# Optimization experiments

Measured on AMD Instinct MI355X. Metric: run time of the kernel, lower is better.

The kernel has to match this reference:

```python
import jax, jax.numpy as jnp
import numpy as np


def setup_inputs() -> dict:
    key = jax.random.key(0)
    ks = jax.random.split(key, 6)
    B, L, N, C, D = 8, 512, 2048, 1024, 128
    return {
        "teacher_logits": jax.random.normal(ks[0], (B, L, N), dtype=jnp.float32),
        "teacher_features": jax.random.normal(ks[1], (B, N, C), dtype=jnp.float32),
        "Wq": jax.random.normal(ks[2], (D, C), dtype=jnp.float32) * (1.0 / np.sqrt(C)),
        "bq": jnp.zeros((D,), dtype=jnp.float32),
        "Wk": jax.random.normal(ks[3], (D, C), dtype=jnp.float32) * (1.0 / np.sqrt(C)),
        "bk": jnp.zeros((D,), dtype=jnp.float32),
    }


def reference(teacher_logits, teacher_features, Wq, bq, Wk, bk):
    # Linear projections (torch nn.Linear: x @ W^T + b)
    query = jnp.einsum("bnc,dc->bnd", teacher_features, Wq) + bq  # [B,N,D]
    key = jnp.einsum("bnc,dc->bnd", teacher_features, Wk) + bk    # [B,N,D]
    energy = jnp.einsum("bnd,bmd->bnm", query, key)               # [B,N,N]
    attention = jax.nn.softmax(energy, axis=-1)                   # softmax over last dim
    # x_m = teacher_logits @ attention^T : [B,L,N] x [B,N,N]^T -> [B,L,N]
    x_m = jnp.einsum("bln,bmn->blm", teacher_logits, attention)
    return x_m
```

## Files before the change

### kernel.cpp

```cpp
#include <hip/hip_runtime.h>
#include <hip/hip_bf16.h>

#define B_ 8
#define L_ 512
#define N_ 2048
#define C_ 1024
#define D_ 128

typedef __attribute__((ext_vector_type(8))) short    short8;
typedef __attribute__((ext_vector_type(4))) short    short4v;
typedef __attribute__((ext_vector_type(8))) _Float16 half8;
typedef __attribute__((ext_vector_type(4))) float    floatx4;

static __device__ __forceinline__ float s2f(short s) {
    return __uint_as_float(((unsigned)(unsigned short)s) << 16);
}
static __device__ __forceinline__ short f2bf(float f) {
    union { __hip_bfloat16 h; short s; } u;
    u.h = __float2bfloat16(f);
    return u.s;
}

struct F8 { float v[8]; };

static __device__ __forceinline__ F8 load8(const void* raw, long off, int is_bf16) {
    F8 r;
    if (is_bf16) {
        short8 x = *reinterpret_cast<const short8*>((const short*)raw + off);
        #pragma unroll
        for (int i = 0; i < 8; ++i) r.v[i] = s2f(x[i]);
    } else {
        const float* p = (const float*)raw + off;
        float4 a = *reinterpret_cast<const float4*>(p);
        float4 b = *reinterpret_cast<const float4*>(p + 4);
        r.v[0]=a.x; r.v[1]=a.y; r.v[2]=a.z; r.v[3]=a.w;
        r.v[4]=b.x; r.v[5]=b.y; r.v[6]=b.z; r.v[7]=b.w;
    }
    return r;
}

static __device__ __forceinline__ float bias_at(const void* raw, int d, int is_bf16) {
    return is_bf16 ? s2f(((const short*)raw)[d]) : ((const float*)raw)[d];
}

static __device__ __forceinline__ void load_lds16(const void* g, void* l) {
    __builtin_amdgcn_global_load_lds(
        (const __attribute__((address_space(1))) void*)g,
        (__attribute__((address_space(3))) void*)l, 16, 0, 0);
}

__global__ void detect_kernel(const unsigned* __restrict__ words, int* __restrict__ flag) {
    int cnt = 0;
    for (int i = threadIdx.x; i < 256; i += 64) {
        float lowv = __uint_as_float(words[i] << 16);
        float a = fabsf(lowv);
        if (a >= 1e-5f && a <= 100.0f) cnt++;
    }
    #pragma unroll
    for (int off = 32; off; off >>= 1) cnt += __shfl_down(cnt, off);
    if (threadIdx.x == 0) flag[0] = (cnt > 128) ? 1 : 0;
}

__global__ __launch_bounds__(256) void cvt_kernel(const void* __restrict__ in_raw,
                                                  short* __restrict__ out, long n,
                                                  const int* __restrict__ flag) {
    if (*flag) return;
    long i = ((long)blockIdx.x * 256 + threadIdx.x) * 8;
    if (i >= n) return;
    F8 x = load8(in_raw, i, 0);
    short8 o;
    #pragma unroll
    for (int j = 0; j < 8; ++j) o[j] = f2bf(x.v[j]);
    *reinterpret_cast<short8*>(out + i) = o;
}

__global__ __launch_bounds__(256) void cvt_half_kernel(const void* __restrict__ in_raw,
                                                       _Float16* __restrict__ out, long n,
                                                       const int* __restrict__ flag) {
    if (*flag) return;
    long i = ((long)blockIdx.x * 256 + threadIdx.x) * 8;
    if (i >= n) return;
    F8 x = load8(in_raw, i, 0);
    half8 o;
    #pragma unroll
    for (int j = 0; j < 8; ++j) o[j] = (_Float16)x.v[j];
    *reinterpret_cast<half8*>(out + i) = o;
}

__global__ __launch_bounds__(512) void proj_kernel(
    const void* __restrict__ Fraw,
    const void* __restrict__ Wq_raw, const void* __restrict__ Wk_raw,
    const _Float16* __restrict__ Wq_h, const _Float16* __restrict__ Wk_h,
    const void* __restrict__ bq_raw, const void* __restrict__ bk_raw,
    _Float16* __restrict__ Q, _Float16* __restrict__ K,
    const int* __restrict__ flag)
{
    const int is_bf16 = *flag;
    const int tid  = threadIdx.x;
    const int wave = tid >> 6;
    const int lane = tid & 63;
    const int quad = lane >> 4;
    const int l16  = lane & 15;
    const long r0  = (long)blockIdx.x * 64;

    const int m0   = (wave & 1) * 32;
    const int col0 = (wave >> 1) * 64;

    __shared__ short Ft[64 * 32];
    __shared__ short Wt[256 * 32];

    floatx4 acc[2][4] = {};

    const int srow = lane >> 2;
    const int sg   = (lane & 3) ^ ((srow >> 1) & 3);
    const int skoff = sg * 8;

    if (is_bf16) {
        const short* Fr  = (const short*)Fraw;
        const short* Wqr = (const short*)Wq_raw;
        const short* Wkr = (const short*)Wk_raw;
        for (int kb = 0; kb < 32; ++kb) {
            const int k0 = kb * 32;
            #pragma unroll
            for (int jj = 0; jj < 2; ++jj) {
                const int c = wave * 2 + jj;
                const short* Wr = (c < 8) ? Wqr : Wkr;
                const int wrow = (c & 7) * 16 + srow;
                load_lds16(Wr + (long)wrow * C_ + k0 + skoff,
                           Wt + c * 512 + lane * 8);
            }
            if (wave < 4) {
                load_lds16(Fr + (r0 + wave * 16 + srow) * (long)C_ + k0 + skoff,
                           Ft + wave * 512 + lane * 8);
            }
            __syncthreads();

            short8 af[2], bfr[4];
            #pragma unroll
            for (int t = 0; t < 2; ++t) {
                const int row = m0 + t * 16 + l16;
                const int ph  = quad ^ ((row >> 1) & 3);
                af[t] = *reinterpret_cast<const short8*>(Ft + row * 32 + ph * 8);
            }
            #pragma unroll
            for (int u = 0; u < 4; ++u) {
                const int wrow = col0 + u * 16 + l16;
                const int ph   = quad ^ ((wrow >> 1) & 3);
                bfr[u] = *reinterpret_cast<const short8*>(Wt + wrow * 32 + ph * 8);
            }
            #pragma unroll
            for (int t = 0; t < 2; ++t)
                #pragma unroll
                for (int u = 0; u < 4; ++u)
                    acc[t][u] = __builtin_amdgcn_mfma_f32_16x16x32_bf16(af[t], bfr[u], acc[t][u], 0, 0, 0);
            __syncthreads();
        }
    } else {
        _Float16* Fth = (_Float16*)Ft;
        _Float16* Wth = (_Float16*)Wt;
        for (int kb = 0; kb < 32; ++kb) {
            const int k0 = kb * 32;
            #pragma unroll
            for (int jj = 0; jj < 2; ++jj) {
                const int c = wave * 2 + jj;
                const _Float16* Wh = (c < 8) ? Wq_h : Wk_h;
                const int wrow = (c & 7) * 16 + srow;
                load_lds16(Wh + (long)wrow * C_ + k0 + skoff,
                           Wth + c * 512 + lane * 8);
            }
            if (tid < 256) {
                const int frow = tid >> 2;
                const int fg   = (tid & 3) ^ ((frow >> 1) & 3);
                F8 x = load8(Fraw, (r0 + frow) * (long)C_ + k0 + fg * 8, 0);
                half8 h;
                #pragma unroll
                for (int j = 0; j < 8; ++j) h[j] = (_Float16)x.v[j];
                *reinterpret_cast<half8*>(Fth + tid * 8) = h;
            }
            __syncthreads();

            half8 af[2], bfr[4];
            #pragma unroll
            for (int t = 0; t < 2; ++t) {
                const int row = m0 + t * 16 + l16;
                const int ph  = quad ^ ((row >> 1) & 3);
                af[t] = *reinterpret_cast<const half8*>(Fth + row * 32 + ph * 8);
            }
            #pragma unroll
            for (int u = 0; u < 4; ++u) {
                const int wrow = col0 + u * 16 + l16;
                const int ph   = quad ^ ((wrow >> 1) & 3);
                bfr[u] = *reinterpret_cast<const half8*>(Wth + wrow * 32 + ph * 8);
            }
            #pragma unroll
            for (int t = 0; t < 2; ++t)
                #pragma unroll
                for (int u = 0; u < 4; ++u)
                    acc[t][u] = __builtin_amdgcn_mfma_f32_16x16x32_f16(af[t], bfr[u], acc[t][u], 0, 0, 0);
            __syncthreads();
        }
    }

    const bool isK = (col0 >= 128);
    const void* braw = isK ? bk_raw : bq_raw;
    _Float16* Out    = isK ? K : Q;
    #pragma unroll
    for (int u = 0; u < 4; ++u) {
        const int d = (col0 + u * 16 + l16) & 127;
        const float bv = bias_at(braw, d, is_bf16);
        #pragma unroll
        for (int t = 0; t < 2; ++t)
            #pragma unroll
            for (int r = 0; r < 4; ++r) {
                const long row = r0 + m0 + t * 16 + quad * 4 + r;
                Out[row * D_ + d] = (_Float16)(acc[t][u][r] + bv);
            }
    }
}

__global__ __launch_bounds__(512, 2) void fused_attn_xm_kernel(
    const void* __restrict__ Lraw,
    const short* __restrict__ Lcvt,
    const _Float16* __restrict__ Q,
    const _Float16* __restrict__ K,
    void* __restrict__ OutRaw,
    const int* __restrict__ flag)
{
    const int is_bf16 = *flag;
    const int f    = blockIdx.y * 32 + blockIdx.x;
    const int b    = f & 7;
    const int m0   = (f >> 3) * 64;
    const int wave = threadIdx.x >> 6;
    const int lane = threadIdx.x & 63;
    const int quad = lane >> 4;
    const int l16  = lane & 15;

    __shared__ short P0[64 * 128];
    __shared__ short P1[64 * 128];
    __shared__ float Zs[64];

    if (threadIdx.x < 64) Zs[threadIdx.x] = 0.0f;

    const short*    Lb = (is_bf16 ? (const short*)Lraw : Lcvt) + (long)b * L_ * N_;
    const _Float16* Qb = Q + (long)b * N_ * D_;
    const _Float16* Kb = K + (long)b * N_ * D_;

    half8 bq[4][4];
    #pragma unroll
    for (int u = 0; u < 4; ++u)
        #pragma unroll
        for (int s = 0; s < 4; ++s)
            bq[u][s] = *reinterpret_cast<const half8*>(
                Qb + (long)(m0 + u * 16 + l16) * D_ + s * 32 + quad * 8);

    const int lw  = wave * 64;
    const int swz = l16 * 2;

    floatx4 acc[4][4] = {};
    float zpart[4] = {};

    #pragma unroll 2
    for (int ch = 0; ch < 16; ++ch) {
        const int n0 = ch * 128;
        short* Pb = (ch & 1) ? P1 : P0;

        const _Float16* krow = Kb + (long)(n0 + wave * 16 + l16) * D_ + quad * 8;
        floatx4 ae[4] = {};
        #pragma unroll
        for (int s = 0; s < 4; ++s) {
            half8 kf = *reinterpret_cast<const half8*>(krow + s * 32);
            #pragma unroll
            for (int u = 0; u < 4; ++u)
                ae[u] = __builtin_amdgcn_mfma_f32_16x16x32_f16(kf, bq[u][s], ae[u], 0, 0, 0);
        }

        short8 al[4][4];
        #pragma unroll
        for (int t = 0; t < 4; ++t)
            #pragma unroll
            for (int ks = 0; ks < 4; ++ks)
                al[t][ks] = *reinterpret_cast<const short8*>(
                    Lb + (long)(lw + t * 16 + l16) * N_ + n0 + ks * 32 + quad * 8);

        #pragma unroll
        for (int u = 0; u < 4; ++u) {
            short4v pk;
            #pragma unroll
            for (int r = 0; r < 4; ++r) {
                float e = __expf(ae[u][r]);
                zpart[u] += e;
                pk[r] = f2bf(e);
            }
            const int m = u * 16 + l16;
            *reinterpret_cast<short4v*>(
                Pb + m * 128 + (((wave * 4 + quad) ^ swz) << 2)) = pk;
        }
        __syncthreads();

        #pragma unroll
        for (int ks = 0; ks < 4; ++ks) {
            short8 bp[4];
            #pragma unroll
            for (int u = 0; u < 4; ++u) {
                const int m = u * 16 + l16;
                bp[u] = *reinterpret_cast<const short8*>(
                    Pb + m * 128 + ((((ks * 8 + quad * 2) ^ swz)) << 2));
            }
            #pragma unroll
            for (int t = 0; t < 4; ++t)
                #pragma unroll
                for (int u = 0; u < 4; ++u)
                    acc[t][u] = __builtin_amdgcn_mfma_f32_16x16x32_bf16(
                        al[t][ks], bp[u], acc[t][u], 0, 0, 0);
        }
    }

    #pragma unroll
    for (int u = 0; u < 4; ++u) {
        float z = zpart[u];
        z += __shfl_xor(z, 16);
        z += __shfl_xor(z, 32);
        if (lane < 16) atomicAdd(&Zs[u * 16 + lane], z);
    }
    __syncthreads();

    float invz[4];
    #pragma unroll
    for (int u = 0; u < 4; ++u) invz[u] = 1.0f / Zs[u * 16 + l16];

    if (is_bf16) {
        short* Ob = (short*)OutRaw + (long)b * L_ * N_;
        #pragma unroll
        for (int t = 0; t < 4; ++t)
            #pragma unroll
            for (int u = 0; u < 4; ++u)
                #pragma unroll
                for (int r = 0; r < 4; ++r) {
                    const long row = lw + t * 16 + quad * 4 + r;
                    const int  col = m0 + u * 16 + l16;
                    Ob[row * N_ + col] = f2bf(acc[t][u][r] * invz[u]);
                }
    } else {
        float* Ob = (float*)OutRaw + (long)b * L_ * N_;
        #pragma unroll
        for (int t = 0; t < 4; ++t)
            #pragma unroll
            for (int u = 0; u < 4; ++u)
                #pragma unroll
                for (int r = 0; r < 4; ++r) {
                    const long row = lw + t * 16 + quad * 4 + r;
                    const int  col = m0 + u * 16 + l16;
                    Ob[row * N_ + col] = acc[t][u][r] * invz[u];
                }
    }
}

extern "C" void kernel_launch(void* const* d_in, const int* in_sizes, int n_in,
                              void* d_out, int out_size, void* d_ws, size_t ws_size,
                              hipStream_t stream) {
    const void* logits_raw = d_in[0];
    const void* feats_raw  = d_in[1];
    const void* wq_raw     = d_in[2];
    const void* bq_raw     = d_in[3];
    const void* wk_raw     = d_in[4];
    const void* bk_raw     = d_in[5];

    char* ws = (char*)d_ws;
    size_t off = 0;
    int* flag = (int*)(ws + off);           off += 256;
    short* logb = (short*)(ws + off);       off += (size_t)B_ * L_ * N_ * 2;
    _Float16* Wq_h = (_Float16*)(ws + off); off += (size_t)D_ * C_ * 2;
    _Float16* Wk_h = (_Float16*)(ws + off); off += (size_t)D_ * C_ * 2;
    _Float16* Q = (_Float16*)(ws + off);    off += (size_t)B_ * N_ * D_ * 2;
    _Float16* K = (_Float16*)(ws + off);    off += (size_t)B_ * N_ * D_ * 2;

    hipLaunchKernelGGL(detect_kernel, dim3(1), dim3(64), 0, stream,
                       (const unsigned*)feats_raw, flag);
    hipLaunchKernelGGL(cvt_kernel, dim3((B_ * L_ * N_) / (256 * 8)), dim3(256), 0, stream,
                       logits_raw, logb, (long)B_ * L_ * N_, flag);
    hipLaunchKernelGGL(cvt_half_kernel, dim3((D_ * C_) / (256 * 8)), dim3(256), 0, stream,
                       wq_raw, Wq_h, (long)D_ * C_, flag);
    hipLaunchKernelGGL(cvt_half_kernel, dim3((D_ * C_) / (256 * 8)), dim3(256), 0, stream,
                       wk_raw, Wk_h, (long)D_ * C_, flag);
    hipLaunchKernelGGL(proj_kernel, dim3(B_ * N_ / 64), dim3(512), 0, stream,
                       feats_raw, wq_raw, wk_raw, Wq_h, Wk_h, bq_raw, bk_raw, Q, K, flag);
    hipLaunchKernelGGL(fused_attn_xm_kernel, dim3(N_ / 64, B_), dim3(512), 0, stream,
                       logits_raw, logb, Q, K, d_out, flag);
}
```

Before: 246.1 us.

## Software-pipeline energy tile computation and stream logits loads per k-step

Restructures the chunk loop so the exp(QK) tile for the next chunk is computed after the current chunk's PV MFMAs and written into the alternate shared buffer, with a prologue for the first chunk. The K rows for the next chunk are prefetched at the top of each iteration. Logits fragments are now loaded one k-step ahead instead of all 16 up front, which lowers register pressure. This trades one fewer barrier on the critical path for more code and a dependence on the compiler scheduling the prefetches well.

```diff
diff --git a/kernel.cpp b/kernel.cpp
--- a/kernel.cpp
+++ b/kernel.cpp
@@ -255,47 +255,55 @@
 
     const int lw  = wave * 64;
     const int swz = l16 * 2;
+    const short* Lw = Lb + (long)(lw + l16) * N_ + quad * 8;
+    const _Float16* Kw = Kb + (long)(wave * 16 + l16) * D_ + quad * 8;
+    const int pwr = ((wave * 4 + quad) ^ swz) << 2;
 
     floatx4 acc[4][4] = {};
     float zpart[4] = {};
+
+    {
+        floatx4 ae[4] = {};
+        #pragma unroll
+        for (int s = 0; s < 4; ++s) {
+            half8 kf = *reinterpret_cast<const half8*>(Kw + s * 32);
+            #pragma unroll
+            for (int u = 0; u < 4; ++u)
+                ae[u] = __builtin_amdgcn_mfma_f32_16x16x32_f16(kf, bq[u][s], ae[u], 0, 0, 0);
+        }
+        #pragma unroll
+        for (int u = 0; u < 4; ++u) {
+            short4v pk;
+            #pragma unroll
+            for (int r = 0; r < 4; ++r) {
+                float e = __expf(ae[u][r]);
+                zpart[u] += e;
+                pk[r] = f2bf(e);
+            }
+            *reinterpret_cast<short4v*>(P0 + (u * 16 + l16) * 128 + pwr) = pk;
+        }
+    }
+    __syncthreads();
 
     #pragma unroll 2
     for (int ch = 0; ch < 16; ++ch) {
         const int n0 = ch * 128;
         short* Pb = (ch & 1) ? P1 : P0;
-
-        const _Float16* krow = Kb + (long)(n0 + wave * 16 + l16) * D_ + quad * 8;
-        floatx4 ae[4] = {};
-        #pragma unroll
-        for (int s = 0; s < 4; ++s) {
-            half8 kf = *reinterpret_cast<const half8*>(krow + s * 32);
-            #pragma unroll
-            for (int u = 0; u < 4; ++u)
-                ae[u] = __builtin_amdgcn_mfma_f32_16x16x32_f16(kf, bq[u][s], ae[u], 0, 0, 0);
-        }
-
-        short8 al[4][4];
+        short* Pn = (ch & 1) ? P0 : P1;
+        const bool notlast = (ch < 15);
+
+        half8 kf[4];
+        if (notlast) {
+            const _Float16* krow = Kw + (long)(n0 + 128) * D_;
+            #pragma unroll
+            for (int s = 0; s < 4; ++s)
+                kf[s] = *reinterpret_cast<const half8*>(krow + s * 32);
+        }
+
+        short8 alv[4];
         #pragma unroll
         for (int t = 0; t < 4; ++t)
-            #pragma unroll
-            for (int ks = 0; ks < 4; ++ks)
-                al[t][ks] = *reinterpret_cast<const short8*>(
-                    Lb + (long)(lw + t * 16 + l16) * N_ + n0 + ks * 32 + quad * 8);
-
-        #pragma unroll
-        for (int u = 0; u < 4; ++u) {
-            short4v pk;
-            #pragma unroll
-            for (int r = 0; r < 4; ++r) {
-                float e = __expf(ae[u][r]);
-                zpart[u] += e;
-                pk[r] = f2bf(e);
-            }
-            const int m = u * 16 + l16;
-            *reinterpret_cast<short4v*>(
-                Pb + m * 128 + (((wave * 4 + quad) ^ swz) << 2)) = pk;
-        }
-        __syncthreads();
+            alv[t] = *reinterpret_cast<const short8*>(Lw + (long)t * 16 * N_ + n0);
 
         #pragma unroll
         for (int ks = 0; ks < 4; ++ks) {
@@ -306,12 +314,42 @@
                 bp[u] = *reinterpret_cast<const short8*>(
                     Pb + m * 128 + ((((ks * 8 + quad * 2) ^ swz)) << 2));
             }
+            short8 aln[4];
+            if (ks < 3) {
+                #pragma unroll
+                for (int t = 0; t < 4; ++t)
+                    aln[t] = *reinterpret_cast<const short8*>(
+                        Lw + (long)t * 16 * N_ + n0 + (ks + 1) * 32);
+            }
             #pragma unroll
             for (int t = 0; t < 4; ++t)
                 #pragma unroll
                 for (int u = 0; u < 4; ++u)
                     acc[t][u] = __builtin_amdgcn_mfma_f32_16x16x32_bf16(
-                        al[t][ks], bp[u], acc[t][u], 0, 0, 0);
+                        alv[t], bp[u], acc[t][u], 0, 0, 0);
+            #pragma unroll
+            for (int t = 0; t < 4; ++t) alv[t] = aln[t];
+        }
+
+        if (notlast) {
+            floatx4 ae[4] = {};
+            #pragma unroll
+            for (int s = 0; s < 4; ++s)
+                #pragma unroll
+                for (int u = 0; u < 4; ++u)
+                    ae[u] = __builtin_amdgcn_mfma_f32_16x16x32_f16(kf[s], bq[u][s], ae[u], 0, 0, 0);
+            #pragma unroll
+            for (int u = 0; u < 4; ++u) {
+                short4v pk;
+                #pragma unroll
+                for (int r = 0; r < 4; ++r) {
+                    float e = __expf(ae[u][r]);
+                    zpart[u] += e;
+                    pk[r] = f2bf(e);
+                }
+                *reinterpret_cast<short4v*>(Pn + (u * 16 + l16) * 128 + pwr) = pk;
+            }
+            __syncthreads();
         }
     }
 
```

After: 254.5 us. 3.4% more time.

## Split fused attention kernel over L halves with 4-wave blocks and pipelined logits loads

Applied to the files above, without the earlier changes.

The fused attention/x_m kernel now uses 256-thread blocks, and each block handles one half of the L dimension, which doubles the grid to 512 blocks. Each wave computes 32 key rows of the energy tile instead of 16, so the per-chunk QK^T work is covered by 4 waves rather than 8. Logits fragments are register double-buffered per k-step, replacing the full 4x4 preload, to cut register pressure and overlap global loads with MFMAs. The trade-off is that every energy/exp computation is now done twice, once per L half, in exchange for more blocks and lower per-thread register use.

```diff
diff --git a/kernel.cpp b/kernel.cpp
--- a/kernel.cpp
+++ b/kernel.cpp
@@ -218,7 +218,7 @@
     }
 }
 
-__global__ __launch_bounds__(512, 2) void fused_attn_xm_kernel(
+__global__ __launch_bounds__(256, 2) void fused_attn_xm_kernel(
     const void* __restrict__ Lraw,
     const short* __restrict__ Lcvt,
     const _Float16* __restrict__ Q,
@@ -227,9 +227,11 @@
     const int* __restrict__ flag)
 {
     const int is_bf16 = *flag;
-    const int f    = blockIdx.y * 32 + blockIdx.x;
+    const int f    = blockIdx.y * 64 + blockIdx.x;
     const int b    = f & 7;
-    const int m0   = (f >> 3) * 64;
+    const int rest = f >> 3;
+    const int m0   = (rest >> 1) * 64;
+    const int l0   = (rest & 1) * 256;
     const int wave = threadIdx.x >> 6;
     const int lane = threadIdx.x & 63;
     const int quad = lane >> 4;
@@ -255,46 +257,53 @@
 
     const int lw  = wave * 64;
     const int swz = l16 * 2;
+    const short* Lw = Lb + (long)(l0 + lw + l16) * N_ + quad * 8;
+    const _Float16* Kw = Kb + (long)(wave * 32 + l16) * D_ + quad * 8;
+    const int pwr0 = (((wave * 2 + 0) * 4 + quad) ^ swz) << 2;
+    const int pwr1 = (((wave * 2 + 1) * 4 + quad) ^ swz) << 2;
 
     floatx4 acc[4][4] = {};
     float zpart[4] = {};
 
-    #pragma unroll 2
     for (int ch = 0; ch < 16; ++ch) {
         const int n0 = ch * 128;
         short* Pb = (ch & 1) ? P1 : P0;
 
-        const _Float16* krow = Kb + (long)(n0 + wave * 16 + l16) * D_ + quad * 8;
-        floatx4 ae[4] = {};
+        const _Float16* krow = Kw + (long)n0 * D_;
+        half8 kf[2][4];
         #pragma unroll
         for (int s = 0; s < 4; ++s) {
-            half8 kf = *reinterpret_cast<const half8*>(krow + s * 32);
-            #pragma unroll
-            for (int u = 0; u < 4; ++u)
-                ae[u] = __builtin_amdgcn_mfma_f32_16x16x32_f16(kf, bq[u][s], ae[u], 0, 0, 0);
+            kf[0][s] = *reinterpret_cast<const half8*>(krow + s * 32);
+            kf[1][s] = *reinterpret_cast<const half8*>(krow + 16 * D_ + s * 32);
         }
-
-        short8 al[4][4];
+        floatx4 ae[2][4] = {};
+        #pragma unroll
+        for (int s = 0; s < 4; ++s)
+            #pragma unroll
+            for (int u = 0; u < 4; ++u) {
+                ae[0][u] = __builtin_amdgcn_mfma_f32_16x16x32_f16(kf[0][s], bq[u][s], ae[0][u], 0, 0, 0);
+                ae[1][u] = __builtin_amdgcn_mfma_f32_16x16x32_f16(kf[1][s], bq[u][s], ae[1][u], 0, 0, 0);
+            }
+
+        short8 alv[4];
         #pragma unroll
         for (int t = 0; t < 4; ++t)
-            #pragma unroll
-            for (int ks = 0; ks < 4; ++ks)
-                al[t][ks] = *reinterpret_cast<const short8*>(
-                    Lb + (long)(lw + t * 16 + l16) * N_ + n0 + ks * 32 + quad * 8);
-
-        #pragma unroll
-        for (int u = 0; u < 4; ++u) {
-            short4v pk;
-            #pragma unroll
-            for (int r = 0; r < 4; ++r) {
-                float e = __expf(ae[u][r]);
-                zpart[u] += e;
-                pk[r] = f2bf(e);
-            }
-            const int m = u * 16 + l16;
-            *reinterpret_cast<short4v*>(
-                Pb + m * 128 + (((wave * 4 + quad) ^ swz) << 2)) = pk;
-        }
+            alv[t] = *reinterpret_cast<const short8*>(Lw + (long)t * 16 * N_ + n0);
+
+        #pragma unroll
+        for (int g = 0; g < 2; ++g)
+            #pragma unroll
+            for (int u = 0; u < 4; ++u) {
+                short4v pk;
+                #pragma unroll
+                for (int r = 0; r < 4; ++r) {
+                    float e = __expf(ae[g][u][r]);
+                    zpart[u] += e;
+                    pk[r] = f2bf(e);
+                }
+                *reinterpret_cast<short4v*>(
+                    Pb + (u * 16 + l16) * 128 + (g ? pwr1 : pwr0)) = pk;
+            }
         __syncthreads();
 
         #pragma unroll
@@ -306,12 +315,21 @@
                 bp[u] = *reinterpret_cast<const short8*>(
                     Pb + m * 128 + ((((ks * 8 + quad * 2) ^ swz)) << 2));
             }
+            short8 aln[4];
+            if (ks < 3) {
+                #pragma unroll
+                for (int t = 0; t < 4; ++t)
+                    aln[t] = *reinterpret_cast<const short8*>(
+                        Lw + (long)t * 16 * N_ + n0 + (ks + 1) * 32);
+            }
             #pragma unroll
             for (int t = 0; t < 4; ++t)
                 #pragma unroll
                 for (int u = 0; u < 4; ++u)
                     acc[t][u] = __builtin_amdgcn_mfma_f32_16x16x32_bf16(
-                        al[t][ks], bp[u], acc[t][u], 0, 0, 0);
+                        alv[t], bp[u], acc[t][u], 0, 0, 0);
+            #pragma unroll
+            for (int t = 0; t < 4; ++t) alv[t] = aln[t];
         }
     }
 
@@ -336,7 +354,7 @@
             for (int u = 0; u < 4; ++u)
                 #pragma unroll
                 for (int r = 0; r < 4; ++r) {
-                    const long row = lw + t * 16 + quad * 4 + r;
+                    const long row = l0 + lw + t * 16 + quad * 4 + r;
                     const int  col = m0 + u * 16 + l16;
                     Ob[row * N_ + col] = f2bf(acc[t][u][r] * invz[u]);
                 }
@@ -348,7 +366,7 @@
             for (int u = 0; u < 4; ++u)
                 #pragma unroll
                 for (int r = 0; r < 4; ++r) {
-                    const long row = lw + t * 16 + quad * 4 + r;
+                    const long row = l0 + lw + t * 16 + quad * 4 + r;
                     const int  col = m0 + u * 16 + l16;
                     Ob[row * N_ + col] = acc[t][u][r] * invz[u];
                 }
@@ -384,6 +402,6 @@
                        wk_raw, Wk_h, (long)D_ * C_, flag);
     hipLaunchKernelGGL(proj_kernel, dim3(B_ * N_ / 64), dim3(512), 0, stream,
                        feats_raw, wq_raw, wk_raw, Wq_h, Wk_h, bq_raw, bk_raw, Q, K, flag);
-    hipLaunchKernelGGL(fused_attn_xm_kernel, dim3(N_ / 64, B_), dim3(512), 0, stream,
+    hipLaunchKernelGGL(fused_attn_xm_kernel, dim3(64, 8), dim3(256), 0, stream,
                        logits_raw, logb, Q, K, d_out, flag);
 }
```

New measurement: 256.7 us. 4.3% more time.

## Double-buffer projection GEMM with wider K tiles, prefetch K, merge weight casts

Applied to the files above, without the earlier changes.

The projection kernel now stages 64-wide K tiles into two LDS buffers and prefetches the next tile while computing on the current one, which halves the number of barrier rounds and hides global load latency. The swizzle changes to an 8-slot XOR pattern to match the wider rows. In the fused attention kernel, the K fragments for the next chunk are loaded ahead of time into registers, and the logits loads are issued before the energy MFMAs. The two weight-cast launches are merged into a single 2D grid launch. In exchange, the projection kernel uses more LDS and the attention kernel holds more registers.

```diff
diff --git a/kernel.cpp b/kernel.cpp
--- a/kernel.cpp
+++ b/kernel.cpp
@@ -74,13 +74,16 @@
     *reinterpret_cast<short8*>(out + i) = o;
 }
 
-__global__ __launch_bounds__(256) void cvt_half_kernel(const void* __restrict__ in_raw,
-                                                       _Float16* __restrict__ out, long n,
-                                                       const int* __restrict__ flag) {
+__global__ __launch_bounds__(256) void cvt_half2_kernel(
+    const void* __restrict__ a_raw, _Float16* __restrict__ a_out,
+    const void* __restrict__ b_raw, _Float16* __restrict__ b_out,
+    long n, const int* __restrict__ flag) {
     if (*flag) return;
+    const void* in  = blockIdx.y ? b_raw : a_raw;
+    _Float16*   out = blockIdx.y ? b_out : a_out;
     long i = ((long)blockIdx.x * 256 + threadIdx.x) * 8;
     if (i >= n) return;
-    F8 x = load8(in_raw, i, 0);
+    F8 x = load8(in, i, 0);
     half8 o;
     #pragma unroll
     for (int j = 0; j < 8; ++j) o[j] = (_Float16)x.v[j];
@@ -106,97 +109,119 @@
     const int m0   = (wave & 1) * 32;
     const int col0 = (wave >> 1) * 64;
 
-    __shared__ short Ft[64 * 32];
-    __shared__ short Wt[256 * 32];
+    __shared__ short Ft[2][64 * 64];
+    __shared__ short Wt[2][256 * 64];
 
     floatx4 acc[2][4] = {};
 
-    const int srow = lane >> 2;
-    const int sg   = (lane & 3) ^ ((srow >> 1) & 3);
-    const int skoff = sg * 8;
+    const int srow  = lane >> 3;
+    const int sslot = lane & 7;
+    const int skoff = (sslot ^ srow) * 8;
 
     if (is_bf16) {
         const short* Fr  = (const short*)Fraw;
         const short* Wqr = (const short*)Wq_raw;
         const short* Wkr = (const short*)Wk_raw;
-        for (int kb = 0; kb < 32; ++kb) {
-            const int k0 = kb * 32;
-            #pragma unroll
-            for (int jj = 0; jj < 2; ++jj) {
-                const int c = wave * 2 + jj;
-                const short* Wr = (c < 8) ? Wqr : Wkr;
-                const int wrow = (c & 7) * 16 + srow;
+
+        auto STAGE = [&](int kb, int buf) {
+            const int k0 = kb * 64;
+            #pragma unroll
+            for (int j = 0; j < 4; ++j) {
+                const int c = wave * 4 + j;
+                const short* Wr = (c < 16) ? Wqr : Wkr;
+                const int wrow = (c & 15) * 8 + srow;
                 load_lds16(Wr + (long)wrow * C_ + k0 + skoff,
-                           Wt + c * 512 + lane * 8);
-            }
-            if (wave < 4) {
-                load_lds16(Fr + (r0 + wave * 16 + srow) * (long)C_ + k0 + skoff,
-                           Ft + wave * 512 + lane * 8);
-            }
-            __syncthreads();
-
-            short8 af[2], bfr[4];
-            #pragma unroll
-            for (int t = 0; t < 2; ++t) {
-                const int row = m0 + t * 16 + l16;
-                const int ph  = quad ^ ((row >> 1) & 3);
-                af[t] = *reinterpret_cast<const short8*>(Ft + row * 32 + ph * 8);
-            }
-            #pragma unroll
-            for (int u = 0; u < 4; ++u) {
-                const int wrow = col0 + u * 16 + l16;
-                const int ph   = quad ^ ((wrow >> 1) & 3);
-                bfr[u] = *reinterpret_cast<const short8*>(Wt + wrow * 32 + ph * 8);
-            }
-            #pragma unroll
-            for (int t = 0; t < 2; ++t)
-                #pragma unroll
-                for (int u = 0; u < 4; ++u)
-                    acc[t][u] = __builtin_amdgcn_mfma_f32_16x16x32_bf16(af[t], bfr[u], acc[t][u], 0, 0, 0);
+                           Wt[buf] + c * 512 + lane * 8);
+            }
+            load_lds16(Fr + (r0 + wave * 8 + srow) * (long)C_ + k0 + skoff,
+                       Ft[buf] + wave * 512 + lane * 8);
+        };
+
+        STAGE(0, 0);
+        __syncthreads();
+        for (int kb = 0; kb < 16; ++kb) {
+            const int buf = kb & 1;
+            if (kb < 15) STAGE(kb + 1, buf ^ 1);
+            #pragma unroll
+            for (int kk = 0; kk < 2; ++kk) {
+                short8 af[2], bfr[4];
+                #pragma unroll
+                for (int t = 0; t < 2; ++t) {
+                    const int row = m0 + t * 16 + l16;
+                    const int ph  = (kk * 4 + quad) ^ (row & 7);
+                    af[t] = *reinterpret_cast<const short8*>(Ft[buf] + row * 64 + ph * 8);
+                }
+                #pragma unroll
+                for (int u = 0; u < 4; ++u) {
+                    const int wrow = col0 + u * 16 + l16;
+                    const int ph   = (kk * 4 + quad) ^ (wrow & 7);
+                    bfr[u] = *reinterpret_cast<const short8*>(Wt[buf] + wrow * 64 + ph * 8);
+                }
+                #pragma unroll
+                for (int t = 0; t < 2; ++t)
+                    #pragma unroll
+                    for (int u = 0; u < 4; ++u)
+                        acc[t][u] = __builtin_amdgcn_mfma_f32_16x16x32_bf16(af[t], bfr[u], acc[t][u], 0, 0, 0);
+            }
             __syncthreads();
         }
     } else {
-        _Float16* Fth = (_Float16*)Ft;
-        _Float16* Wth = (_Float16*)Wt;
-        for (int kb = 0; kb < 32; ++kb) {
-            const int k0 = kb * 32;
-            #pragma unroll
-            for (int jj = 0; jj < 2; ++jj) {
-                const int c = wave * 2 + jj;
-                const _Float16* Wh = (c < 8) ? Wq_h : Wk_h;
-                const int wrow = (c & 7) * 16 + srow;
+        _Float16* FtH0 = (_Float16*)Ft[0];
+        _Float16* FtH1 = (_Float16*)Ft[1];
+        _Float16* WtH0 = (_Float16*)Wt[0];
+        _Float16* WtH1 = (_Float16*)Wt[1];
+
+        const int frow = tid >> 3;
+        const int fseg = tid & 7;
+        const int fph  = fseg ^ (frow & 7);
+
+        auto STAGE = [&](int kb, int buf) {
+            const int k0 = kb * 64;
+            _Float16* Wth = buf ? WtH1 : WtH0;
+            _Float16* Fth = buf ? FtH1 : FtH0;
+            #pragma unroll
+            for (int j = 0; j < 4; ++j) {
+                const int c = wave * 4 + j;
+                const _Float16* Wh = (c < 16) ? Wq_h : Wk_h;
+                const int wrow = (c & 15) * 8 + srow;
                 load_lds16(Wh + (long)wrow * C_ + k0 + skoff,
                            Wth + c * 512 + lane * 8);
             }
-            if (tid < 256) {
-                const int frow = tid >> 2;
-                const int fg   = (tid & 3) ^ ((frow >> 1) & 3);
-                F8 x = load8(Fraw, (r0 + frow) * (long)C_ + k0 + fg * 8, 0);
-                half8 h;
-                #pragma unroll
-                for (int j = 0; j < 8; ++j) h[j] = (_Float16)x.v[j];
-                *reinterpret_cast<half8*>(Fth + tid * 8) = h;
-            }
-            __syncthreads();
-
-            half8 af[2], bfr[4];
-            #pragma unroll
-            for (int t = 0; t < 2; ++t) {
-                const int row = m0 + t * 16 + l16;
-                const int ph  = quad ^ ((row >> 1) & 3);
-                af[t] = *reinterpret_cast<const half8*>(Fth + row * 32 + ph * 8);
-            }
-            #pragma unroll
-            for (int u = 0; u < 4; ++u) {
-                const int wrow = col0 + u * 16 + l16;
-                const int ph   = quad ^ ((wrow >> 1) & 3);
-                bfr[u] = *reinterpret_cast<const half8*>(Wth + wrow * 32 + ph * 8);
-            }
-            #pragma unroll
-            for (int t = 0; t < 2; ++t)
-                #pragma unroll
-                for (int u = 0; u < 4; ++u)
-                    acc[t][u] = __builtin_amdgcn_mfma_f32_16x16x32_f16(af[t], bfr[u], acc[t][u], 0, 0, 0);
+            F8 x = load8(Fraw, (r0 + frow) * (long)C_ + k0 + fseg * 8, 0);
+            half8 h;
+            #pragma unroll
+            for (int j = 0; j < 8; ++j) h[j] = (_Float16)x.v[j];
+            *reinterpret_cast<half8*>(Fth + frow * 64 + fph * 8) = h;
+        };
+
+        STAGE(0, 0);
+        __syncthreads();
+        for (int kb = 0; kb < 16; ++kb) {
+            const int buf = kb & 1;
+            if (kb < 15) STAGE(kb + 1, buf ^ 1);
+            _Float16* Wth = buf ? WtH1 : WtH0;
+            _Float16* Fth = buf ? FtH1 : FtH0;
+            #pragma unroll
+            for (int kk = 0; kk < 2; ++kk) {
+                half8 af[2], bfr[4];
+                #pragma unroll
+                for (int t = 0; t < 2; ++t) {
+                    const int row = m0 + t * 16 + l16;
+                    const int ph  = (kk * 4 + quad) ^ (row & 7);
+                    af[t] = *reinterpret_cast<const half8*>(Fth + row * 64 + ph * 8);
+                }
+                #pragma unroll
+                for (int u = 0; u < 4; ++u) {
+                    const int wrow = col0 + u * 16 + l16;
+                    const int ph   = (kk * 4 + quad) ^ (wrow & 7);
+                    bfr[u] = *reinterpret_cast<const half8*>(Wth + wrow * 64 + ph * 8);
+                }
+                #pragma unroll
+                for (int t = 0; t < 2; ++t)
+                    #pragma unroll
+                    for (int u = 0; u < 4; ++u)
+                        acc[t][u] = __builtin_amdgcn_mfma_f32_16x16x32_f16(af[t], bfr[u], acc[t][u], 0, 0, 0);
+            }
             __syncthreads();
         }
     }
@@ -255,32 +280,44 @@
 
     const int lw  = wave * 64;
     const int swz = l16 * 2;
+    const short* Lw = Lb + (long)(lw + l16) * N_ + quad * 8;
+    const _Float16* Kw = Kb + (long)(wave * 16 + l16) * D_ + quad * 8;
+    const int pwr = ((wave * 4 + quad) ^ swz) << 2;
 
     floatx4 acc[4][4] = {};
     float zpart[4] = {};
+
+    half8 kf[4];
+    #pragma unroll
+    for (int s = 0; s < 4; ++s)
+        kf[s] = *reinterpret_cast<const half8*>(Kw + s * 32);
 
     #pragma unroll 2
     for (int ch = 0; ch < 16; ++ch) {
         const int n0 = ch * 128;
         short* Pb = (ch & 1) ? P1 : P0;
 
-        const _Float16* krow = Kb + (long)(n0 + wave * 16 + l16) * D_ + quad * 8;
-        floatx4 ae[4] = {};
-        #pragma unroll
-        for (int s = 0; s < 4; ++s) {
-            half8 kf = *reinterpret_cast<const half8*>(krow + s * 32);
-            #pragma unroll
-            for (int u = 0; u < 4; ++u)
-                ae[u] = __builtin_amdgcn_mfma_f32_16x16x32_f16(kf, bq[u][s], ae[u], 0, 0, 0);
-        }
-
         short8 al[4][4];
         #pragma unroll
         for (int t = 0; t < 4; ++t)
             #pragma unroll
             for (int ks = 0; ks < 4; ++ks)
                 al[t][ks] = *reinterpret_cast<const short8*>(
-                    Lb + (long)(lw + t * 16 + l16) * N_ + n0 + ks * 32 + quad * 8);
+                    Lw + (long)t * 16 * N_ + n0 + ks * 32);
+
+        floatx4 ae[4] = {};
+        #pragma unroll
+        for (int s = 0; s < 4; ++s)
+            #pragma unroll
+            for (int u = 0; u < 4; ++u)
+                ae[u] = __builtin_amdgcn_mfma_f32_16x16x32_f16(kf[s], bq[u][s], ae[u], 0, 0, 0);
+
+        if (ch < 15) {
+            const _Float16* krow = Kw + (long)(n0 + 128) * D_;
+            #pragma unroll
+            for (int s = 0; s < 4; ++s)
+                kf[s] = *reinterpret_cast<const half8*>(krow + s * 32);
+        }
 
         #pragma unroll
         for (int u = 0; u < 4; ++u) {
@@ -291,9 +328,7 @@
                 zpart[u] += e;
                 pk[r] = f2bf(e);
             }
-            const int m = u * 16 + l16;
-            *reinterpret_cast<short4v*>(
-                Pb + m * 128 + (((wave * 4 + quad) ^ swz) << 2)) = pk;
+            *reinterpret_cast<short4v*>(Pb + (u * 16 + l16) * 128 + pwr) = pk;
         }
         __syncthreads();
 
@@ -378,10 +413,8 @@
                        (const unsigned*)feats_raw, flag);
     hipLaunchKernelGGL(cvt_kernel, dim3((B_ * L_ * N_) / (256 * 8)), dim3(256), 0, stream,
                        logits_raw, logb, (long)B_ * L_ * N_, flag);
-    hipLaunchKernelGGL(cvt_half_kernel, dim3((D_ * C_) / (256 * 8)), dim3(256), 0, stream,
-                       wq_raw, Wq_h, (long)D_ * C_, flag);
-    hipLaunchKernelGGL(cvt_half_kernel, dim3((D_ * C_) / (256 * 8)), dim3(256), 0, stream,
-                       wk_raw, Wk_h, (long)D_ * C_, flag);
+    hipLaunchKernelGGL(cvt_half2_kernel, dim3((D_ * C_) / (256 * 8), 2), dim3(256), 0, stream,
+                       wq_raw, Wq_h, wk_raw, Wk_h, (long)D_ * C_, flag);
     hipLaunchKernelGGL(proj_kernel, dim3(B_ * N_ / 64), dim3(512), 0, stream,
                        feats_raw, wq_raw, wk_raw, Wq_h, Wk_h, bq_raw, bk_raw, Q, K, flag);
     hipLaunchKernelGGL(fused_attn_xm_kernel, dim3(N_ / 64, B_), dim3(512), 0, stream,
```

Measured after the change: 281.0 us. 14.1% more time.
